# Performance work log

Hardware: AMD Instinct MI355X
Metric: run time of the kernel (lower is better)

Reference implementation:

```python
import jax, jax.numpy as jnp
import numpy as np
from jax.scipy.special import logsumexp

BS, SEQ, DM = 4, 4096, 1024
H, HD = 16, 64
BLK = 128
NB = SEQ // BLK          # 32 blocks
MAX_NB = 32
N_ITERS = 5
TEMP = 1.0
CLIP = 1.0


def setup_inputs() -> dict:
    key = jax.random.key(0)
    ks = jax.random.split(key, 12)
    s = 0.02
    return {
        'inputs_q': jax.random.normal(ks[0], (BS, SEQ, DM), jnp.float32),
        'wq': jax.random.normal(ks[1], (DM, H, HD), jnp.float32) * s,
        'bq': jnp.zeros((H, HD), jnp.float32),
        'wk': jax.random.normal(ks[2], (DM, H, HD), jnp.float32) * s,
        'bk': jnp.zeros((H, HD), jnp.float32),
        'wv': jax.random.normal(ks[3], (DM, H, HD), jnp.float32) * s,
        'bv': jnp.zeros((H, HD), jnp.float32),
        'w_sort': jax.random.normal(ks[4], (H, HD, MAX_NB), jnp.float32) * s,
        'b_sort': jnp.zeros((MAX_NB,), jnp.float32),
        'wo': jax.random.normal(ks[5], (H, HD, DM), jnp.float32) * s,
        'bo': jnp.zeros((DM,), jnp.float32),
    }


def sinkhorn_operator(log_alpha, n_iters=N_ITERS, temp=TEMP, clip=CLIP):
    # non-causal path of the original: iterative row/col log-normalization
    n = log_alpha.shape[1]
    la = jnp.reshape(log_alpha, (-1, n, n)) / temp
    for _ in range(n_iters):
        la = la - logsumexp(la, axis=2, keepdims=True)  # row normalize
        la = la - logsumexp(la, axis=1, keepdims=True)  # col normalize
    return jnp.exp(jnp.clip(la, -clip, clip))


def reference(inputs_q, wq, bq, wk, bk, wv, bv, w_sort, b_sort, wo, bo):
    bs, qlen, _ = inputs_q.shape
    nb = qlen // BLK
    # QKV projections: (bs, seq, H, HD)
    q = jnp.einsum('bsf,fhd->bshd', inputs_q, wq) + bq
    k = jnp.einsum('bsf,fhd->bshd', inputs_q, wk) + bk  # self-attention: inputs_kv = inputs_q
    v = jnp.einsum('bsf,fhd->bshd', inputs_q, wv) + bv
    # block reshape: (bs, nb, BLK, H, HD)
    qb = q.reshape(bs, nb, BLK, H, HD)
    kb = k.reshape(bs, nb, BLK, H, HD)
    vb = v.reshape(bs, nb, BLK, H, HD)
    # sort network: pool keys within block, project (H,HD)->MAX_NB
    sum_key = jnp.sum(kb, axis=2)                                   # (bs, nb, H, HD)
    sort_out = jnp.einsum('bnhd,hdm->bnm', sum_key, w_sort) + b_sort
    sort_mat = sort_out[:, :, :nb]                                  # (bs, nb, nb)
    perm = sinkhorn_operator(sort_mat)                              # (bs, nb, nb)
    # soft block sorting of keys/values
    sorted_k = jnp.einsum('bnm,bmshd->bnshd', perm, kb)
    sorted_v = jnp.einsum('bnm,bmshd->bnshd', perm, vb)
    # attend within each block to [local kv ; sorted kv]
    kcat = jnp.concatenate([kb, sorted_k], axis=2)                  # (bs, nb, 2BLK, H, HD)
    vcat = jnp.concatenate([vb, sorted_v], axis=2)
    scale = 1.0 / jnp.sqrt(jnp.float32(HD))
    logits = jnp.einsum('bnqhd,bnkhd->bnhqk', qb * scale, kcat)     # (bs, nb, H, BLK, 2BLK)
    w = jax.nn.softmax(logits, axis=-1)
    x = jnp.einsum('bnhqk,bnkhd->bnqhd', w, vcat)                   # (bs, nb, BLK, H, HD)
    x = x.reshape(bs, qlen, H, HD)
    return jnp.einsum('bshd,hdf->bsf', x, wo) + bo
```

## Files before the change

kernel.cpp:

```cpp
#include <hip/hip_runtime.h>
#include <stdint.h>

typedef short bf16x8 __attribute__((ext_vector_type(8)));
typedef float f32x4 __attribute__((ext_vector_type(4)));
typedef unsigned short u16;
typedef unsigned short u16x4 __attribute__((ext_vector_type(4)));

#define AS1 __attribute__((address_space(1)))
#define AS3 __attribute__((address_space(3)))

__device__ __forceinline__ void gll16(const void* g, void* l) {
  __builtin_amdgcn_global_load_lds((const AS1 uint32_t*)g, (AS3 uint32_t*)l, 16, 0, 0);
}

__device__ __forceinline__ f32x4 mfma16(bf16x8 a, bf16x8 b, f32x4 c) {
  return __builtin_amdgcn_mfma_f32_16x16x32_bf16(a, b, c, 0, 0, 0);
}

__device__ __forceinline__ u16 f2bf(float f) {
  union { float f; uint32_t u; } c; c.f = f;
  uint32_t r = c.u + 0x7FFFu + ((c.u >> 16) & 1u);
  return (u16)(r >> 16);
}
__device__ __forceinline__ float bf2f(u16 h) {
  union { uint32_t u; float f; } c; c.u = ((uint32_t)h) << 16; return c.f;
}

__global__ __launch_bounds__(256) void k_cast(const float* __restrict__ in, u16* __restrict__ out) {
  int i = (blockIdx.x * 256 + threadIdx.x) * 4;
  float4 v = *(const float4*)(in + i);
  u16x4 r; r.x = f2bf(v.x); r.y = f2bf(v.y); r.z = f2bf(v.z); r.w = f2bf(v.w);
  *(u16x4*)(out + i) = r;
}

__global__ __launch_bounds__(1024) void k_transpose4(
    const float* __restrict__ wq, const float* __restrict__ wk,
    const float* __restrict__ wv, const float* __restrict__ wo,
    u16* __restrict__ Wqkvt, u16* __restrict__ Wot) {
  __shared__ float t[32][33];
  const float* src; u16* dst;
  int z = blockIdx.z;
  if (z == 0)      { src = wq; dst = Wqkvt; }
  else if (z == 1) { src = wk; dst = Wqkvt + 1024 * 1024; }
  else if (z == 2) { src = wv; dst = Wqkvt + 2 * 1024 * 1024; }
  else             { src = wo; dst = Wot; }
  int tx = threadIdx.x, ty = threadIdx.y;
  t[ty][tx] = src[(size_t)(blockIdx.y * 32 + ty) * 1024 + blockIdx.x * 32 + tx];
  __syncthreads();
  dst[(size_t)(blockIdx.x * 32 + ty) * 1024 + blockIdx.y * 32 + tx] = f2bf(t[tx][ty]);
}

__device__ __forceinline__ void gemm256_loop(
    const u16* __restrict__ Ag, const u16* __restrict__ Bg,
    u16* lds, int m0, int n0, f32x4 (&acc)[8][4])
{
  const int tid = threadIdx.x, lane = tid & 63, w = tid >> 6;
  const int wm = w >> 2, wn = w & 3;
  const int l8 = lane >> 3, c7 = lane & 7;
  const int mm = lane & 15, quad = lane >> 4;
  const int ch0 = (quad ^ (mm & 7)) * 8;
  const int ch1 = ((quad ^ (mm & 7)) ^ 4) * 8;

  const u16* aSt = Ag + (size_t)(m0 + w * 8 + l8) * 1024 + (c7 ^ l8) * 8;
  const u16* bSt = Bg + (size_t)(n0 + w * 8 + l8) * 1024 + (c7 ^ l8) * 8;
  u16* ldsAw = lds + w * 512;
  u16* ldsBw = lds + 32768 + w * 512;
  const u16* aR0 = lds + (wm * 128 + mm) * 64 + ch0;
  const u16* aR1 = lds + (wm * 128 + mm) * 64 + ch1;
  const u16* bR0 = lds + 32768 + (wn * 64 + mm) * 64 + ch0;
  const u16* bR1 = lds + 32768 + (wn * 64 + mm) * 64 + ch1;

#define STA(q, kt, buf) gll16(aSt + (q) * 65536 + (kt) * 64, ldsAw + (buf) * 16384 + (q) * 4096)
#define STB(q, kt, buf) gll16(bSt + (q) * 65536 + (kt) * 64, ldsBw + (buf) * 16384 + (q) * 4096)

#define LDA(C, MH) do {                                                                  \
    _Pragma("unroll")                                                                    \
    for (int i = 0; i < 4; ++i) {                                                        \
      af[i][0] = *(const bf16x8*)(aR0 + (C) * 16384 + ((MH) * 64 + i * 16) * 64);        \
      af[i][1] = *(const bf16x8*)(aR1 + (C) * 16384 + ((MH) * 64 + i * 16) * 64);        \
    }                                                                                    \
  } while (0)
#define LDBv(C, NH, DST) do {                                                            \
    _Pragma("unroll")                                                                    \
    for (int j = 0; j < 2; ++j) {                                                        \
      DST[j][0] = *(const bf16x8*)(bR0 + (C) * 16384 + ((NH) * 32 + j * 16) * 64);       \
      DST[j][1] = *(const bf16x8*)(bR1 + (C) * 16384 + ((NH) * 32 + j * 16) * 64);       \
    }                                                                                    \
  } while (0)
#define MM(MH, NH, BF) do {                                                              \
    __builtin_amdgcn_s_setprio(1);                                                       \
    _Pragma("unroll")                                                                    \
    for (int ks = 0; ks < 2; ++ks)                                                       \
      _Pragma("unroll")                                                                  \
      for (int i = 0; i < 4; ++i)                                                        \
        _Pragma("unroll")                                                                \
        for (int j = 0; j < 2; ++j)                                                      \
          acc[(MH) * 4 + i][(NH) * 2 + j] =                                              \
              mfma16(af[i][ks], BF[j][ks], acc[(MH) * 4 + i][(NH) * 2 + j]);             \
    __builtin_amdgcn_s_setprio(0);                                                       \
  } while (0)

#define TILE(TT, C) do {                                                                 \
    const int t1 = (TT) + 1, t2 = (TT) + 2;                                              \
    const bool sB = t1 < 16, sA = t2 < 16;                                               \
                                                                                \
    LDA(C, 0); LDBv(C, 0, bfA);                                                          \
    __builtin_amdgcn_sched_barrier(0);            \
    LDBv(C, 1, bfB);                                                                     \
    __builtin_amdgcn_sched_barrier(0);                                                   \
    if (sB) { STB(0, t1, 1 - (C)); STB(1, t1, 1 - (C)); }                                \
    asm volatile("s_waitcnt lgkmcnt(4)" ::: "memory");             \
    __builtin_amdgcn_sched_barrier(0);                                                   \
    MM(0, 0, bfA);                                                                       \
                                        \
    if (sB) { STB(2, t1, 1 - (C)); STB(3, t1, 1 - (C)); }                                \
    asm volatile("s_waitcnt lgkmcnt(0)" ::: "memory");            \
    __builtin_amdgcn_sched_barrier(0);                                                   \
    MM(0, 1, bfB);                                                                       \
                                                                                \
    LDA(C, 1);                                       \
    __builtin_amdgcn_sched_barrier(0);                                                   \
    asm volatile("s_waitcnt lgkmcnt(0)" ::: "memory");                 \
    __builtin_amdgcn_sched_barrier(0);                                                   \
    MM(1, 1, bfB);                                                                       \
    __builtin_amdgcn_s_barrier();                                                \
                                                                                \
    if (sA) { STA(0, t2, C); STA(1, t2, C); STA(2, t2, C); STA(3, t2, C); }              \
    MM(1, 0, bfA);                                                                       \
    if ((TT) < 14)       asm volatile("s_waitcnt vmcnt(4)" ::: "memory");                \
    else if ((TT) == 14) asm volatile("s_waitcnt vmcnt(0)" ::: "memory");                \
    __builtin_amdgcn_s_barrier();                                                \
  } while (0)

#pragma unroll
  for (int i = 0; i < 8; ++i)
#pragma unroll
    for (int j = 0; j < 4; ++j) acc[i][j] = (f32x4){0.f, 0.f, 0.f, 0.f};

  STA(0, 0, 0); STA(1, 0, 0); STA(2, 0, 0); STA(3, 0, 0);
  STB(0, 0, 0); STB(1, 0, 0); STB(2, 0, 0); STB(3, 0, 0);
  STA(0, 1, 1); STA(1, 1, 1); STA(2, 1, 1); STA(3, 1, 1);
  asm volatile("s_waitcnt vmcnt(4)" ::: "memory");
  __builtin_amdgcn_s_barrier();

#pragma unroll 1
  for (int t = 0; t < 16; t += 2) {
    bf16x8 af[4][2]; bf16x8 bfA[2][2]; bf16x8 bfB[2][2];
    TILE(t, 0);
    TILE(t + 1, 1);
  }
#undef TILE
#undef MM
#undef LDA
#undef LDBv
#undef STA
#undef STB
}

__global__ __launch_bounds__(512, 2) void k_gemm_qkv(
    const u16* __restrict__ A, const u16* __restrict__ Bt,
    const float* __restrict__ bq, const float* __restrict__ bk, const float* __restrict__ bv,
    u16* __restrict__ Qb, u16* __restrict__ Kb, u16* __restrict__ Vbt, float* __restrict__ sumk)
{
  __shared__ __align__(16) u16 LDS[65536];
  int lin = blockIdx.x + 12 * blockIdx.y;
  int nb = (lin & 7) * 96 + (lin >> 3);
  const int m0 = (nb / 12) * 256, n0 = (nb % 12) * 256;
  f32x4 acc[8][4];
  gemm256_loop(A, Bt, LDS, m0, n0, acc);

  const int tid = threadIdx.x, lane = tid & 63, w = tid >> 6;
  const int wm = w >> 2, wn = w & 3;
  const int mm = lane & 15, quad = lane >> 4;
  const int sel = n0 >> 10;
  const float* bias = sel == 0 ? bq : (sel == 1 ? bk : bv);
  u16* W = LDS + w * 8192;

  if (sel == 2) {
#pragma unroll
    for (int nf = 0; nf < 4; ++nf) {
      int d = nf * 16 + mm;
      float bval = bias[((n0 & 1023) + wn * 64 + nf * 16 + mm)];
#pragma unroll
      for (int mf = 0; mf < 8; ++mf) {
        int c = mf * 4 + quad;
        u16x4 pk;
        pk.x = f2bf(acc[mf][nf][0] + bval);
        pk.y = f2bf(acc[mf][nf][1] + bval);
        pk.z = f2bf(acc[mf][nf][2] + bval);
        pk.w = f2bf(acc[mf][nf][3] + bval);
        *(u16x4*)(W + d * 128 + (c ^ (d & 15)) * 4) = pk;
      }
    }
    asm volatile("s_waitcnt lgkmcnt(0)" ::: "memory");
    int h_w = ((n0 & 1023) >> 6) + wn;
    int b_ = m0 >> 12;
    int c = lane & 31, dpar = lane >> 5;
    size_t gbase = ((size_t)(b_ * 16 + h_w) * 64) * 4096 + (m0 & 4095) + wm * 128 + c * 4;
#pragma unroll
    for (int dd = 0; dd < 32; ++dd) {
      int d = dd * 2 + dpar;
      u16x4 v = *(const u16x4*)(W + d * 128 + (c ^ (d & 15)) * 4);
      *(u16x4*)(Vbt + gbase + (size_t)d * 4096) = v;
    }
    return;
  }

  const float scl = sel == 0 ? 0.125f : 1.0f;
#pragma unroll
  for (int nf = 0; nf < 4; ++nf) {
    float bval = bias[(n0 & 1023) + wn * 64 + nf * 16 + mm];
    int d = nf * 16 + mm;
    int dc = d >> 3, dw = d & 7;
#pragma unroll
    for (int mf = 0; mf < 8; ++mf)
#pragma unroll
      for (int r = 0; r < 4; ++r) {
        int s = mf * 16 + quad * 4 + r;
        int kk = (s ^ (s >> 3)) & 7;
        W[s * 64 + ((dc ^ kk) << 3) + dw] = f2bf((acc[mf][nf][r] + bval) * scl);
      }
  }
  asm volatile("s_waitcnt lgkmcnt(0)" ::: "memory");
  {
    int h = ((n0 & 1023) >> 6) + wn;
    int mg0 = m0 + wm * 128;
    int b_ = mg0 >> 12;
    u16* dst = (sel == 0 ? Qb : Kb) + ((size_t)(b_ * 16 + h) * 4096 + (mg0 & 4095)) * 64;
    int l8 = lane >> 3, c8 = lane & 7;
#pragma unroll
    for (int i = 0; i < 16; ++i) {
      int s = i * 8 + l8;
      int kk = (l8 ^ i) & 7;
      *(bf16x8*)(dst + s * 64 + c8 * 8) = *(const bf16x8*)(W + s * 64 + ((c8 ^ kk) << 3));
    }
  }

  if (sel == 1) {
#pragma unroll
    for (int nf = 0; nf < 4; ++nf) {
      float ssum = 0.f;
#pragma unroll
      for (int mf = 0; mf < 8; ++mf)
#pragma unroll
        for (int r = 0; r < 4; ++r) ssum += acc[mf][nf][r];
      ssum += __shfl_xor(ssum, 16);
      ssum += __shfl_xor(ssum, 32);
      if (quad == 0) {
        int colg = (n0 - 1024) + wn * 64 + nf * 16 + mm;
        int b_ = m0 >> 12, nb2 = ((m0 >> 7) & 31) + wm;
        sumk[(size_t)(b_ * 32 + nb2) * 1024 + colg] = ssum + 128.f * bias[colg];
      }
    }
  }
}

__global__ __launch_bounds__(512, 2) void k_gemm_out(
    const u16* __restrict__ A, const u16* __restrict__ Bt,
    const float* __restrict__ bo, float* __restrict__ out)
{
  __shared__ __align__(16) u16 LDS[65536];
  int lin = blockIdx.x + 4 * blockIdx.y;
  int nb = (lin & 7) * 32 + (lin >> 3);
  const int m0 = (nb / 4) * 256, n0 = (nb % 4) * 256;
  f32x4 acc[8][4];
  gemm256_loop(A, Bt, LDS, m0, n0, acc);

  const int tid = threadIdx.x, lane = tid & 63, w = tid >> 6;
  const int wm = w >> 2, wn = w & 3;
  const int mm = lane & 15, quad = lane >> 4;
#pragma unroll
  for (int nf = 0; nf < 4; ++nf) {
    int ng = n0 + wn * 64 + nf * 16 + mm;
    float bval = bo[ng];
#pragma unroll
    for (int mf = 0; mf < 8; ++mf)
#pragma unroll
      for (int r = 0; r < 4; ++r) {
        int mg = m0 + wm * 128 + mf * 16 + quad * 4 + r;
        out[(size_t)mg * 1024 + ng] = acc[mf][nf][r] + bval;
      }
  }
}

__global__ __launch_bounds__(256) void k_sortmm(const float* __restrict__ sumk, const float* __restrict__ wsort,
                                                const float* __restrict__ bsort, float* __restrict__ so) {
  __shared__ float red[256];
  int n = blockIdx.x, b = blockIdx.y, t = threadIdx.x;
  int m = t & 31, kp = t >> 5;
  const float* row = sumk + (size_t)(b * 32 + n) * 1024;
  float acc = 0.f;
  for (int c = kp * 128; c < kp * 128 + 128; ++c) acc += row[c] * wsort[c * 32 + m];
  red[t] = acc;
  __syncthreads();
  if (t < 32) {
    float s = bsort[t];
#pragma unroll
    for (int q = 0; q < 8; ++q) s += red[q * 32 + t];
    so[(size_t)(b * 32 + n) * 32 + t] = s;
  }
}

__global__ __launch_bounds__(32) void k_sinkhorn(const float* __restrict__ so, float* __restrict__ perm) {
  __shared__ float A[32][33];
  int b = blockIdx.x, t = threadIdx.x;
  for (int i = 0; i < 32; ++i) A[i][t] = so[(size_t)(b * 32 + i) * 32 + t];
  __syncthreads();
  for (int it = 0; it < 5; ++it) {
    {
      float mx = -1e30f;
      for (int j = 0; j < 32; ++j) mx = fmaxf(mx, A[t][j]);
      float s = 0.f;
      for (int j = 0; j < 32; ++j) s += __expf(A[t][j] - mx);
      float l = mx + __logf(s);
      for (int j = 0; j < 32; ++j) A[t][j] -= l;
    }
    __syncthreads();
    {
      float mx = -1e30f;
      for (int j = 0; j < 32; ++j) mx = fmaxf(mx, A[j][t]);
      float s = 0.f;
      for (int j = 0; j < 32; ++j) s += __expf(A[j][t] - mx);
      float l = mx + __logf(s);
      for (int j = 0; j < 32; ++j) A[j][t] -= l;
    }
    __syncthreads();
  }
  for (int i = 0; i < 32; ++i)
    perm[(size_t)(b * 32 + i) * 32 + t] = __expf(fminf(fmaxf(A[i][t], -1.f), 1.f));
}

__global__ __launch_bounds__(256) void k_mix(
    const u16* __restrict__ Kb, const u16* __restrict__ Vbt, const float* __restrict__ perm,
    u16* __restrict__ Ksort, u16* __restrict__ Vsort)
{
  __shared__ float P[32][32];
  int b = blockIdx.z, y = blockIdx.y, xg = blockIdx.x;
  int tid = threadIdx.x;
#pragma unroll
  for (int i = 0; i < 4; ++i) {
    int idx = i * 256 + tid;
    P[idx >> 5][idx & 31] = perm[b * 1024 + idx];
  }
  __syncthreads();
  if (y < 16) {
    int h = y;
    int ss = xg * 4 + (tid >> 6), d = tid & 63;
    const u16* Kg = Kb + (size_t)(b * 16 + h) * 262144;
    float xk[32];
#pragma unroll
    for (int m = 0; m < 32; ++m) xk[m] = bf2f(Kg[(size_t)(m * 128 + ss) * 64 + d]);
    size_t tbase = (size_t)((b * 16 + h) * 32) * 8192;
#pragma unroll
    for (int nn = 0; nn < 32; ++nn) {
      float sk = 0.f;
#pragma unroll
      for (int m4 = 0; m4 < 8; ++m4) {
        float4 pv = *(const float4*)&P[nn][m4 * 4];
        sk += pv.x * xk[m4 * 4 + 0] + pv.y * xk[m4 * 4 + 1] + pv.z * xk[m4 * 4 + 2] + pv.w * xk[m4 * 4 + 3];
      }
      Ksort[tbase + (size_t)nn * 8192 + ss * 64 + d] = f2bf(sk);
    }
  } else {
    int h = y - 16;
    int d = xg * 2 + (tid >> 7), ss = tid & 127;
    const u16* Vg = Vbt + ((size_t)(b * 16 + h) * 64 + d) * 4096;
    float xv[32];
#pragma unroll
    for (int m = 0; m < 32; ++m) xv[m] = bf2f(Vg[m * 128 + ss]);
    size_t tbase = (size_t)((b * 16 + h) * 32) * 8192;
#pragma unroll
    for (int nn = 0; nn < 32; ++nn) {
      float sv = 0.f;
#pragma unroll
      for (int m4 = 0; m4 < 8; ++m4) {
        float4 pv = *(const float4*)&P[nn][m4 * 4];
        sv += pv.x * xv[m4 * 4 + 0] + pv.y * xv[m4 * 4 + 1] + pv.z * xv[m4 * 4 + 2] + pv.w * xv[m4 * 4 + 3];
      }
      Vsort[tbase + (size_t)nn * 8192 + d * 128 + ss] = f2bf(sv);
    }
  }
}

__global__ __launch_bounds__(256, 2) void k_attn(
    const u16* __restrict__ Qb, const u16* __restrict__ Kb, const u16* __restrict__ Ksort,
    const u16* __restrict__ Vbt, const u16* __restrict__ Vsort, u16* __restrict__ X)
{
  __shared__ u16 Ks[16384];
  __shared__ u16 Vlo[8192];
  __shared__ u16 Vhi[8192];
  int tid = threadIdx.x, lane = tid & 63, w = tid >> 6;
  int n = blockIdx.x, h = blockIdx.y, b = blockIdx.z;
  size_t bh = (size_t)(b * 16 + h);
  size_t tileK = bh * 32 + n;

  {
    int l8 = lane >> 3, sl8 = lane & 7;
    const u16* Korig = Kb + (bh * 4096 + (size_t)n * 128) * 64;
    const u16* Ksrt  = Ksort + tileK * 8192;
#pragma unroll
    for (int c = 0; c < 8; ++c) {
      int cc = w * 8 + c;
      int r = cc * 8 + l8;
      int pk = sl8 ^ (r & 7);
      const u16* src = (cc < 16) ? (Korig + (size_t)r * 64 + pk * 8)
                                 : (Ksrt + (size_t)(r - 128) * 64 + pk * 8);
      gll16(src, Ks + cc * 512);
    }
    int l16 = lane >> 4, sl16 = lane & 15;
    const u16* Vorig = Vbt + bh * 262144 + (size_t)n * 128;
    const u16* Vsrt  = Vsort + tileK * 8192;
#pragma unroll
    for (int c = 0; c < 4; ++c) {
      int cc = w * 4 + c;
      int d = cc * 4 + l16;
      int pv = sl16 ^ (d & 15);
      gll16(Vorig + (size_t)d * 4096 + pv * 8, Vlo + cc * 512);
      gll16(Vsrt + (size_t)d * 128 + pv * 8, Vhi + cc * 512);
    }
  }

  int mm = lane & 15, quad = lane >> 4;
  bf16x8 qf[2][2];
  {
    size_t qrow = bh * 4096 + n * 128 + w * 32;
#pragma unroll
    for (int mt = 0; mt < 2; ++mt)
#pragma unroll
      for (int ks = 0; ks < 2; ++ks)
        qf[mt][ks] = *(const bf16x8*)(Qb + (qrow + mt * 16 + mm) * 64 + ks * 32 + quad * 8);
  }
  __syncthreads();

  f32x4 S[2][16];
#pragma unroll
  for (int mt = 0; mt < 2; ++mt)
#pragma unroll
    for (int nt = 0; nt < 16; ++nt) S[mt][nt] = (f32x4){0.f, 0.f, 0.f, 0.f};
#pragma unroll
  for (int nt = 0; nt < 16; ++nt) {
    int kk = nt * 16 + mm;
#pragma unroll
    for (int ks = 0; ks < 2; ++ks) {
      int ch = (ks * 4 + quad) ^ (kk & 7);
      bf16x8 bk = *(const bf16x8*)(Ks + kk * 64 + ch * 8);
      S[0][nt] = mfma16(qf[0][ks], bk, S[0][nt]);
      S[1][nt] = mfma16(qf[1][ks], bk, S[1][nt]);
    }
  }

  float mx[2][4], ls[2][4];
#pragma unroll
  for (int mt = 0; mt < 2; ++mt)
#pragma unroll
    for (int r = 0; r < 4; ++r) {
      float v = S[mt][0][r];
#pragma unroll
      for (int nt = 1; nt < 16; ++nt) v = fmaxf(v, S[mt][nt][r]);
#pragma unroll
      for (int o = 1; o < 16; o <<= 1) v = fmaxf(v, __shfl_xor(v, o));
      mx[mt][r] = v;
    }
#pragma unroll
  for (int mt = 0; mt < 2; ++mt)
#pragma unroll
    for (int nt = 0; nt < 16; ++nt)
#pragma unroll
      for (int r = 0; r < 4; ++r)
        S[mt][nt][r] = __expf(S[mt][nt][r] - mx[mt][r]);
#pragma unroll
  for (int mt = 0; mt < 2; ++mt)
#pragma unroll
    for (int r = 0; r < 4; ++r) {
      float s = 0.f;
#pragma unroll
      for (int nt = 0; nt < 16; ++nt) s += S[mt][nt][r];
#pragma unroll
      for (int o = 1; o < 16; o <<= 1) s += __shfl_xor(s, o);
      ls[mt][r] = s;
    }

  __syncthreads();

  u16* Pw = Ks + w * 4096;
  f32x4 O[2][4];
#pragma unroll
  for (int mt = 0; mt < 2; ++mt)
#pragma unroll
    for (int dt = 0; dt < 4; ++dt) O[mt][dt] = (f32x4){0.f, 0.f, 0.f, 0.f};

#pragma unroll
  for (int half = 0; half < 2; ++half) {
    const u16* Vp = half == 0 ? Vlo : Vhi;
#pragma unroll
    for (int mt = 0; mt < 2; ++mt)
#pragma unroll
      for (int nt8 = 0; nt8 < 8; ++nt8) {
        int nt = half * 8 + nt8;
        int kkl = nt8 * 16 + mm;
#pragma unroll
        for (int r = 0; r < 4; ++r) {
          int q = mt * 16 + quad * 4 + r;
          int ch = (kkl >> 3) ^ (q & 15);
          Pw[q * 128 + ch * 8 + (kkl & 7)] = f2bf(S[mt][nt][r]);
        }
      }
#pragma unroll
    for (int ksl = 0; ksl < 4; ++ksl) {
      bf16x8 pa[2];
#pragma unroll
      for (int mt = 0; mt < 2; ++mt) {
        int q = mt * 16 + mm;
        int ch = (ksl * 4 + quad) ^ (q & 15);
        pa[mt] = *(const bf16x8*)(Pw + q * 128 + ch * 8);
      }
#pragma unroll
      for (int dt = 0; dt < 4; ++dt) {
        int d = dt * 16 + mm;
        int ch = (ksl * 4 + quad) ^ (d & 15);
        bf16x8 vb = *(const bf16x8*)(Vp + d * 128 + ch * 8);
        O[0][dt] = mfma16(pa[0], vb, O[0][dt]);
        O[1][dt] = mfma16(pa[1], vb, O[1][dt]);
      }
    }
  }

#pragma unroll
  for (int mt = 0; mt < 2; ++mt)
#pragma unroll
    for (int dt = 0; dt < 4; ++dt)
#pragma unroll
      for (int r = 0; r < 4; ++r) {
        int q = w * 32 + mt * 16 + quad * 4 + r;
        float val = O[mt][dt][r] / ls[mt][r];
        size_t row = (size_t)b * 4096 + n * 128 + q;
        X[row * 1024 + h * 64 + dt * 16 + mm] = f2bf(val);
      }
}

extern "C" void kernel_launch(void* const* d_in, const int* in_sizes, int n_in,
                              void* d_out, int out_size, void* d_ws, size_t ws_size,
                              hipStream_t stream) {
  const float* inq   = (const float*)d_in[0];
  const float* wq    = (const float*)d_in[1];
  const float* bq    = (const float*)d_in[2];
  const float* wk    = (const float*)d_in[3];
  const float* bk    = (const float*)d_in[4];
  const float* wv    = (const float*)d_in[5];
  const float* bv    = (const float*)d_in[6];
  const float* wsort = (const float*)d_in[7];
  const float* bsort = (const float*)d_in[8];
  const float* wo    = (const float*)d_in[9];
  const float* bo    = (const float*)d_in[10];
  float* out = (float*)d_out;

  char* ws = (char*)d_ws;
  size_t off = 0;
  auto alloc = [&](size_t bytes) { char* p = ws + off; off += (bytes + 255) & ~(size_t)255; return p; };
  u16*  Qb    = (u16*)alloc(33554432);
  u16*  Kb    = (u16*)alloc(33554432);
  u16*  Vbt   = (u16*)alloc(33554432);
  u16*  Ksort = (u16*)alloc(33554432);
  u16*  Vsort = (u16*)alloc(33554432);
  u16*  Abf   = (u16*)alloc(33554432);
  u16*  Wqkvt = (u16*)alloc(6291456);
  u16*  Wot   = (u16*)alloc(2097152);
  float* sumk = (float*)alloc(524288);
  float* so   = (float*)alloc(16384);
  float* perm = (float*)alloc(16384);
  u16*  X = Abf;

  k_cast<<<16384, 256, 0, stream>>>(inq, Abf);
  k_transpose4<<<dim3(32, 32, 4), dim3(32, 32), 0, stream>>>(wq, wk, wv, wo, Wqkvt, Wot);
  k_gemm_qkv<<<dim3(12, 64), 512, 0, stream>>>(Abf, Wqkvt, bq, bk, bv, Qb, Kb, Vbt, sumk);
  k_sortmm<<<dim3(32, 4), 256, 0, stream>>>(sumk, wsort, bsort, so);
  k_sinkhorn<<<4, 32, 0, stream>>>(so, perm);
  k_mix<<<dim3(32, 32, 4), 256, 0, stream>>>(Kb, Vbt, perm, Ksort, Vsort);
  k_attn<<<dim3(32, 16, 4), 256, 0, stream>>>(Qb, Kb, Ksort, Vbt, Vsort, X);
  k_gemm_out<<<dim3(4, 64), 512, 0, stream>>>(X, Wot, bo, out);
}
```

Measured before the change: 428.8 us.

## Fuse sort projection with Sinkhorn, vectorize mix kernel, stage attention output via LDS

Merges the sort-network matvec and the Sinkhorn normalization into one 4-block kernel, removing one launch and the intermediate buffer. The mix kernel now has each thread handle 4 contiguous elements using 8-byte vector loads and stores, with a quarter of the grid. The attention epilogue multiplies by a reciprocal, writes the output tile into swizzled LDS, then stores 16-byte rows to X. The price is a serial 1024-long dot product per thread in only 4 blocks, and more registers in the mix kernel.

```diff
diff --git a/kernel.cpp b/kernel.cpp
--- a/kernel.cpp
+++ b/kernel.cpp
@@ -283,31 +283,29 @@
   }
 }
 
-__global__ __launch_bounds__(256) void k_sortmm(const float* __restrict__ sumk, const float* __restrict__ wsort,
-                                                const float* __restrict__ bsort, float* __restrict__ so) {
-  __shared__ float red[256];
-  int n = blockIdx.x, b = blockIdx.y, t = threadIdx.x;
-  int m = t & 31, kp = t >> 5;
-  const float* row = sumk + (size_t)(b * 32 + n) * 1024;
-  float acc = 0.f;
-  for (int c = kp * 128; c < kp * 128 + 128; ++c) acc += row[c] * wsort[c * 32 + m];
-  red[t] = acc;
-  __syncthreads();
-  if (t < 32) {
-    float s = bsort[t];
-#pragma unroll
-    for (int q = 0; q < 8; ++q) s += red[q * 32 + t];
-    so[(size_t)(b * 32 + n) * 32 + t] = s;
-  }
-}
-
-__global__ __launch_bounds__(32) void k_sinkhorn(const float* __restrict__ so, float* __restrict__ perm) {
+__global__ __launch_bounds__(256) void k_sortsink(
+    const float* __restrict__ sumk, const float* __restrict__ wsort,
+    const float* __restrict__ bsort, float* __restrict__ perm) {
   __shared__ float A[32][33];
   int b = blockIdx.x, t = threadIdx.x;
-  for (int i = 0; i < 32; ++i) A[i][t] = so[(size_t)(b * 32 + i) * 32 + t];
+  {
+    int n = t >> 3, mg = t & 7;
+    const float* row = sumk + (size_t)(b * 32 + n) * 1024;
+    float a0 = 0.f, a1 = 0.f, a2 = 0.f, a3 = 0.f;
+#pragma unroll 4
+    for (int c = 0; c < 1024; ++c) {
+      float s = row[c];
+      float4 w4 = *(const float4*)(wsort + c * 32 + mg * 4);
+      a0 += s * w4.x; a1 += s * w4.y; a2 += s * w4.z; a3 += s * w4.w;
+    }
+    A[n][mg * 4 + 0] = a0 + bsort[mg * 4 + 0];
+    A[n][mg * 4 + 1] = a1 + bsort[mg * 4 + 1];
+    A[n][mg * 4 + 2] = a2 + bsort[mg * 4 + 2];
+    A[n][mg * 4 + 3] = a3 + bsort[mg * 4 + 3];
+  }
   __syncthreads();
   for (int it = 0; it < 5; ++it) {
-    {
+    if (t < 32) {
       float mx = -1e30f;
       for (int j = 0; j < 32; ++j) mx = fmaxf(mx, A[t][j]);
       float s = 0.f;
@@ -316,7 +314,7 @@
       for (int j = 0; j < 32; ++j) A[t][j] -= l;
     }
     __syncthreads();
-    {
+    if (t < 32) {
       float mx = -1e30f;
       for (int j = 0; j < 32; ++j) mx = fmaxf(mx, A[j][t]);
       float s = 0.f;
@@ -326,8 +324,11 @@
     }
     __syncthreads();
   }
-  for (int i = 0; i < 32; ++i)
-    perm[(size_t)(b * 32 + i) * 32 + t] = __expf(fminf(fmaxf(A[i][t], -1.f), 1.f));
+#pragma unroll
+  for (int i = 0; i < 4; ++i) {
+    int idx = i * 256 + t;
+    perm[(size_t)b * 1024 + idx] = __expf(fminf(fmaxf(A[idx >> 5][idx & 31], -1.f), 1.f));
+  }
 }
 
 __global__ __launch_bounds__(256) void k_mix(
@@ -345,39 +346,47 @@
   __syncthreads();
   if (y < 16) {
     int h = y;
-    int ss = xg * 4 + (tid >> 6), d = tid & 63;
+    int ss = xg * 16 + (tid >> 4), dq = (tid & 15) * 4;
     const u16* Kg = Kb + (size_t)(b * 16 + h) * 262144;
-    float xk[32];
-#pragma unroll
-    for (int m = 0; m < 32; ++m) xk[m] = bf2f(Kg[(size_t)(m * 128 + ss) * 64 + d]);
+    float xk[32][4];
+#pragma unroll
+    for (int m = 0; m < 32; ++m) {
+      u16x4 v = *(const u16x4*)(Kg + (size_t)(m * 128 + ss) * 64 + dq);
+      xk[m][0] = bf2f(v.x); xk[m][1] = bf2f(v.y); xk[m][2] = bf2f(v.z); xk[m][3] = bf2f(v.w);
+    }
     size_t tbase = (size_t)((b * 16 + h) * 32) * 8192;
-#pragma unroll
+#pragma unroll 1
     for (int nn = 0; nn < 32; ++nn) {
-      float sk = 0.f;
-#pragma unroll
-      for (int m4 = 0; m4 < 8; ++m4) {
-        float4 pv = *(const float4*)&P[nn][m4 * 4];
-        sk += pv.x * xk[m4 * 4 + 0] + pv.y * xk[m4 * 4 + 1] + pv.z * xk[m4 * 4 + 2] + pv.w * xk[m4 * 4 + 3];
-      }
-      Ksort[tbase + (size_t)nn * 8192 + ss * 64 + d] = f2bf(sk);
+      float s0 = 0.f, s1 = 0.f, s2 = 0.f, s3 = 0.f;
+#pragma unroll
+      for (int m = 0; m < 32; ++m) {
+        float p = P[nn][m];
+        s0 += p * xk[m][0]; s1 += p * xk[m][1]; s2 += p * xk[m][2]; s3 += p * xk[m][3];
+      }
+      u16x4 o; o.x = f2bf(s0); o.y = f2bf(s1); o.z = f2bf(s2); o.w = f2bf(s3);
+      *(u16x4*)(Ksort + tbase + (size_t)nn * 8192 + ss * 64 + dq) = o;
     }
   } else {
     int h = y - 16;
-    int d = xg * 2 + (tid >> 7), ss = tid & 127;
+    int d = xg * 8 + (tid >> 5), sq = (tid & 31) * 4;
     const u16* Vg = Vbt + ((size_t)(b * 16 + h) * 64 + d) * 4096;
-    float xv[32];
-#pragma unroll
-    for (int m = 0; m < 32; ++m) xv[m] = bf2f(Vg[m * 128 + ss]);
+    float xv[32][4];
+#pragma unroll
+    for (int m = 0; m < 32; ++m) {
+      u16x4 v = *(const u16x4*)(Vg + m * 128 + sq);
+      xv[m][0] = bf2f(v.x); xv[m][1] = bf2f(v.y); xv[m][2] = bf2f(v.z); xv[m][3] = bf2f(v.w);
+    }
     size_t tbase = (size_t)((b * 16 + h) * 32) * 8192;
-#pragma unroll
+#pragma unroll 1
     for (int nn = 0; nn < 32; ++nn) {
-      float sv = 0.f;
-#pragma unroll
-      for (int m4 = 0; m4 < 8; ++m4) {
-        float4 pv = *(const float4*)&P[nn][m4 * 4];
-        sv += pv.x * xv[m4 * 4 + 0] + pv.y * xv[m4 * 4 + 1] + pv.z * xv[m4 * 4 + 2] + pv.w * xv[m4 * 4 + 3];
-      }
-      Vsort[tbase + (size_t)nn * 8192 + d * 128 + ss] = f2bf(sv);
+      float s0 = 0.f, s1 = 0.f, s2 = 0.f, s3 = 0.f;
+#pragma unroll
+      for (int m = 0; m < 32; ++m) {
+        float p = P[nn][m];
+        s0 += p * xv[m][0]; s1 += p * xv[m][1]; s2 += p * xv[m][2]; s3 += p * xv[m][3];
+      }
+      u16x4 o; o.x = f2bf(s0); o.y = f2bf(s1); o.z = f2bf(s2); o.w = f2bf(s3);
+      *(u16x4*)(Vsort + tbase + (size_t)nn * 8192 + d * 128 + sq) = o;
     }
   }
 }
@@ -468,6 +477,7 @@
 #pragma unroll
       for (int r = 0; r < 4; ++r)
         S[mt][nt][r] = __expf(S[mt][nt][r] - mx[mt][r]);
+  float rls[2][4];
 #pragma unroll
   for (int mt = 0; mt < 2; ++mt)
 #pragma unroll
@@ -478,6 +488,7 @@
 #pragma unroll
       for (int o = 1; o < 16; o <<= 1) s += __shfl_xor(s, o);
       ls[mt][r] = s;
+      rls[mt][r] = 1.0f / s;
     }
 
   __syncthreads();
@@ -531,11 +542,23 @@
     for (int dt = 0; dt < 4; ++dt)
 #pragma unroll
       for (int r = 0; r < 4; ++r) {
-        int q = w * 32 + mt * 16 + quad * 4 + r;
-        float val = O[mt][dt][r] / ls[mt][r];
-        size_t row = (size_t)b * 4096 + n * 128 + q;
-        X[row * 1024 + h * 64 + dt * 16 + mm] = f2bf(val);
-      }
+        int q = mt * 16 + quad * 4 + r;
+        int d = dt * 16 + mm;
+        int kk = (q ^ (q >> 3)) & 7;
+        Pw[q * 64 + (((d >> 3) ^ kk) << 3) + (d & 7)] = f2bf(O[mt][dt][r] * rls[mt][r]);
+      }
+  asm volatile("s_waitcnt lgkmcnt(0)" ::: "memory");
+  {
+    size_t row0 = (size_t)b * 4096 + n * 128 + w * 32;
+    int l8 = lane >> 3, c8 = lane & 7;
+#pragma unroll
+    for (int i = 0; i < 4; ++i) {
+      int s = i * 8 + l8;
+      int kk = (l8 ^ i) & 7;
+      *(bf16x8*)(X + (row0 + s) * 1024 + h * 64 + c8 * 8) =
+          *(const bf16x8*)(Pw + s * 64 + ((c8 ^ kk) << 3));
+    }
+  }
 }
 
 extern "C" void kernel_launch(void* const* d_in, const int* in_sizes, int n_in,
@@ -566,16 +589,14 @@
   u16*  Wqkvt = (u16*)alloc(6291456);
   u16*  Wot   = (u16*)alloc(2097152);
   float* sumk = (float*)alloc(524288);
-  float* so   = (float*)alloc(16384);
   float* perm = (float*)alloc(16384);
   u16*  X = Abf;
 
   k_cast<<<16384, 256, 0, stream>>>(inq, Abf);
   k_transpose4<<<dim3(32, 32, 4), dim3(32, 32), 0, stream>>>(wq, wk, wv, wo, Wqkvt, Wot);
   k_gemm_qkv<<<dim3(12, 64), 512, 0, stream>>>(Abf, Wqkvt, bq, bk, bv, Qb, Kb, Vbt, sumk);
-  k_sortmm<<<dim3(32, 4), 256, 0, stream>>>(sumk, wsort, bsort, so);
-  k_sinkhorn<<<4, 32, 0, stream>>>(so, perm);
-  k_mix<<<dim3(32, 32, 4), 256, 0, stream>>>(Kb, Vbt, perm, Ksort, Vsort);
+  k_sortsink<<<4, 256, 0, stream>>>(sumk, wsort, bsort, perm);
+  k_mix<<<dim3(8, 32, 4), 256, 0, stream>>>(Kb, Vbt, perm, Ksort, Vsort);
   k_attn<<<dim3(32, 16, 4), 256, 0, stream>>>(Qb, Kb, Ksort, Vbt, Vsort, X);
   k_gemm_out<<<dim3(4, 64), 512, 0, stream>>>(X, Wot, bo, out);
 }
```

After: 486.5 us. 1.13x slower.
